# Kernel optimization log

Hardware: AMD Instinct MI355X
Metric: run time of the kernel (lower is better)

## Reference

```python
import jax, jax.numpy as jnp
import numpy as np
import math

D_MODEL = 1024
N_HEADS = 16
HEAD_DIM = D_MODEL // N_HEADS
TOP_K = 32
SCALE = math.sqrt(HEAD_DIM)


def setup_inputs() -> dict:
    key = jax.random.key(0)
    ks = jax.random.split(key, 12)
    B, S, N = 2, 2048, 2048
    std = 1.0 / math.sqrt(D_MODEL)
    inp = {
        "x": jax.random.normal(ks[0], (B, S, D_MODEL), dtype=jnp.float32),
        "knowledge_embeddings": jax.random.normal(ks[1], (B, N, D_MODEL), dtype=jnp.float32),
        "Wq": jax.random.normal(ks[2], (D_MODEL, D_MODEL), dtype=jnp.float32) * std,
        "bq": jnp.zeros((D_MODEL,), dtype=jnp.float32),
        "Wk": jax.random.normal(ks[3], (D_MODEL, D_MODEL), dtype=jnp.float32) * std,
        "bk": jnp.zeros((D_MODEL,), dtype=jnp.float32),
        "Wv": jax.random.normal(ks[4], (D_MODEL, D_MODEL), dtype=jnp.float32) * std,
        "bv": jnp.zeros((D_MODEL,), dtype=jnp.float32),
        "Wo": jax.random.normal(ks[5], (D_MODEL, D_MODEL), dtype=jnp.float32) * std,
        "bo": jnp.zeros((D_MODEL,), dtype=jnp.float32),
    }
    return inp


def _split_heads(t, n):
    # [B, L, d_model] -> [B, H, L, head_dim]
    B, L, _ = t.shape
    return t.reshape(B, L, N_HEADS, HEAD_DIM).transpose(0, 2, 1, 3)


def reference(x, knowledge_embeddings, Wq, bq, Wk, bk, Wv, bv, Wo, bo):
    B, S, _ = x.shape
    N = knowledge_embeddings.shape[1]
    Q = _split_heads(x @ Wq.T + bq, N_HEADS)                    # [B,H,S,hd]
    K = _split_heads(knowledge_embeddings @ Wk.T + bk, N_HEADS)  # [B,H,N,hd]
    V = _split_heads(knowledge_embeddings @ Wv.T + bv, N_HEADS)  # [B,H,N,hd]

    scores = jnp.einsum("bhsd,bhnd->bhsn", Q, K) / SCALE        # [B,H,S,N]
    k = min(TOP_K, N)
    topk_scores, topk_indices = jax.lax.top_k(scores, k)        # [B,H,S,k]
    sparse_weights = jax.nn.softmax(topk_scores, axis=-1)       # [B,H,S,k]
    # dropout=0.0 (eval) -> identity

    # gather V rows: V [B,H,N,hd] with indices [B,H,S,k] along N axis
    sel_V = jnp.take_along_axis(
        V[:, :, None, :, :],                  # [B,H,1,N,hd]
        topk_indices[..., None],              # [B,H,S,k,1]
        axis=3,
    )                                          # [B,H,S,k,hd]
    context = jnp.einsum("bhsk,bhskd->bhsd", sparse_weights, sel_V)
    context = context.transpose(0, 2, 1, 3).reshape(B, S, D_MODEL)
    return context @ Wo.T + bo
```

## Files before the change

kernel.cpp:

```cpp
#include <hip/hip_runtime.h>
#include <math.h>

typedef unsigned long long u64;
typedef unsigned int u32;
typedef unsigned short ush;
typedef __attribute__((ext_vector_type(8))) short short8;
typedef __attribute__((ext_vector_type(4))) float f32x4;

#define BATCH   2
#define SEQ     2048
#define NKNOW   2048
#define DMODEL  1024
#define NHEADS  16
#define HDIM    64
#define TOPK    32
#define MSEL    44

#define MFMA16(A, B, C) __builtin_amdgcn_mfma_f32_16x16x32_bf16(A, B, C, 0, 0, 0)

__device__ __forceinline__ ush f2bf(float x) {
    u32 u = __float_as_uint(x);
    return (ush)((u + 0x7FFFu + ((u >> 16) & 1u)) >> 16);
}
__device__ __forceinline__ float bf2f(ush b) { return __uint_as_float(((u32)b) << 16); }

__global__ __launch_bounds__(256) void gemm_xwt_bias(
    const float* __restrict__ X, const float* __restrict__ W,
    const float* __restrict__ bias, float* __restrict__ Y)
{
    __shared__ float As[16][132];
    __shared__ float Bs[16][132];

    const int t  = threadIdx.x;
    const int m0 = blockIdx.x * 128;
    const int n0 = blockIdx.y * 128;

    const int lm = t >> 2;
    const int lk = (t & 3) << 2;
    const int tx = t & 15;
    const int ty = t >> 4;

    float acc[8][8];
#pragma unroll
    for (int i = 0; i < 8; ++i)
#pragma unroll
        for (int j = 0; j < 8; ++j) acc[i][j] = 0.f;

    for (int k0 = 0; k0 < 1024; k0 += 16) {
        float4 a0 = *(const float4*)(X + (size_t)(m0 + lm) * 1024 + k0 + lk);
        float4 a1 = *(const float4*)(X + (size_t)(m0 + lm + 64) * 1024 + k0 + lk);
        float4 b0 = *(const float4*)(W + (size_t)(n0 + lm) * 1024 + k0 + lk);
        float4 b1 = *(const float4*)(W + (size_t)(n0 + lm + 64) * 1024 + k0 + lk);
        __syncthreads();
        As[lk + 0][lm] = a0.x; As[lk + 1][lm] = a0.y; As[lk + 2][lm] = a0.z; As[lk + 3][lm] = a0.w;
        As[lk + 0][lm + 64] = a1.x; As[lk + 1][lm + 64] = a1.y; As[lk + 2][lm + 64] = a1.z; As[lk + 3][lm + 64] = a1.w;
        Bs[lk + 0][lm] = b0.x; Bs[lk + 1][lm] = b0.y; Bs[lk + 2][lm] = b0.z; Bs[lk + 3][lm] = b0.w;
        Bs[lk + 0][lm + 64] = b1.x; Bs[lk + 1][lm + 64] = b1.y; Bs[lk + 2][lm + 64] = b1.z; Bs[lk + 3][lm + 64] = b1.w;
        __syncthreads();
#pragma unroll
        for (int k = 0; k < 16; ++k) {
            float a[8], b[8];
            *(float4*)(a)     = *(const float4*)&As[k][ty * 8];
            *(float4*)(a + 4) = *(const float4*)&As[k][ty * 8 + 4];
            *(float4*)(b)     = *(const float4*)&Bs[k][tx * 4];
            *(float4*)(b + 4) = *(const float4*)&Bs[k][64 + tx * 4];
#pragma unroll
            for (int i = 0; i < 8; ++i)
#pragma unroll
                for (int j = 0; j < 8; ++j)
                    acc[i][j] = fmaf(a[i], b[j], acc[i][j]);
        }
    }

    float4 bv0 = *(const float4*)(bias + n0 + tx * 4);
    float4 bv1 = *(const float4*)(bias + n0 + 64 + tx * 4);
#pragma unroll
    for (int i = 0; i < 8; ++i) {
        size_t row = (size_t)(m0 + ty * 8 + i) * 1024;
        float4 r0, r1;
        r0.x = acc[i][0] + bv0.x; r0.y = acc[i][1] + bv0.y;
        r0.z = acc[i][2] + bv0.z; r0.w = acc[i][3] + bv0.w;
        r1.x = acc[i][4] + bv1.x; r1.y = acc[i][5] + bv1.y;
        r1.z = acc[i][6] + bv1.z; r1.w = acc[i][7] + bv1.w;
        *(float4*)(Y + row + n0 + tx * 4)      = r0;
        *(float4*)(Y + row + n0 + 64 + tx * 4) = r1;
    }
}

__global__ __launch_bounds__(256) void split_bf16(
    const float* __restrict__ in, ush* __restrict__ oh, ush* __restrict__ ol, int n)
{
    int i = (blockIdx.x * 256 + threadIdx.x) * 4;
    if (i >= n) return;
    float4 v = *(const float4*)(in + i);
    ush h0 = f2bf(v.x), h1 = f2bf(v.y), h2 = f2bf(v.z), h3 = f2bf(v.w);
    ushort4 hv; hv.x = h0; hv.y = h1; hv.z = h2; hv.w = h3;
    ushort4 lv;
    lv.x = f2bf(v.x - bf2f(h0)); lv.y = f2bf(v.y - bf2f(h1));
    lv.z = f2bf(v.z - bf2f(h2)); lv.w = f2bf(v.w - bf2f(h3));
    *(ushort4*)(oh + i) = hv;
    *(ushort4*)(ol + i) = lv;
}

__global__ __launch_bounds__(256) void conv_bf16(
    const float* __restrict__ in, ush* __restrict__ o, int n)
{
    int i = (blockIdx.x * 256 + threadIdx.x) * 4;
    if (i >= n) return;
    float4 v = *(const float4*)(in + i);
    ushort4 hv;
    hv.x = f2bf(v.x); hv.y = f2bf(v.y); hv.z = f2bf(v.z); hv.w = f2bf(v.w);
    *(ushort4*)(o + i) = hv;
}

__global__ __launch_bounds__(256) void gemm_mfma_split(
    const ush* __restrict__ Ah, const ush* __restrict__ Al,
    const ush* __restrict__ Bh, const ush* __restrict__ Bl,
    const float* __restrict__ bias, float* __restrict__ Yf)
{
    __shared__ ush sAh[4096], sAl[4096];
    __shared__ ush sBh[8192], sBl[8192];

    const int t = threadIdx.x;
    const int w = t >> 6, lane = t & 63;
    const int m0 = blockIdx.x * 64;
    const int n0 = blockIdx.y * 128;

    f32x4 acc[4][2];
#pragma unroll
    for (int i = 0; i < 4; ++i)
#pragma unroll
        for (int j = 0; j < 2; ++j) acc[i][j] = (f32x4){0.f, 0.f, 0.f, 0.f};

    for (int k0 = 0; k0 < 1024; k0 += 64) {
        __syncthreads();
#pragma unroll
        for (int c = t; c < 512; c += 256) {
            int t16 = c >> 7, ks = (c >> 6) & 1, ln = c & 63;
            int row = t16 * 16 + (ln & 15);
            int k8  = ks * 4 + (ln >> 4);
            size_t g = (size_t)(m0 + row) * 1024 + k0 + k8 * 8;
            *(uint4*)&sAh[c * 8] = *(const uint4*)(Ah + g);
            *(uint4*)&sAl[c * 8] = *(const uint4*)(Al + g);
        }
#pragma unroll
        for (int c = t; c < 1024; c += 256) {
            int t16 = c >> 7, ks = (c >> 6) & 1, ln = c & 63;
            int row = t16 * 16 + (ln & 15);
            int k8  = ks * 4 + (ln >> 4);
            size_t g = (size_t)(n0 + row) * 1024 + k0 + k8 * 8;
            *(uint4*)&sBh[c * 8] = *(const uint4*)(Bh + g);
            *(uint4*)&sBl[c * 8] = *(const uint4*)(Bl + g);
        }
        __syncthreads();

#pragma unroll
        for (int ks = 0; ks < 2; ++ks) {
            short8 a_h[4], a_l[4], b_h[2], b_l[2];
#pragma unroll
            for (int i = 0; i < 4; ++i) {
                a_h[i] = *(const short8*)&sAh[((i * 2 + ks) * 64 + lane) * 8];
                a_l[i] = *(const short8*)&sAl[((i * 2 + ks) * 64 + lane) * 8];
            }
#pragma unroll
            for (int j = 0; j < 2; ++j) {
                int nt = w * 2 + j;
                b_h[j] = *(const short8*)&sBh[((nt * 2 + ks) * 64 + lane) * 8];
                b_l[j] = *(const short8*)&sBl[((nt * 2 + ks) * 64 + lane) * 8];
            }
#pragma unroll
            for (int i = 0; i < 4; ++i)
#pragma unroll
                for (int j = 0; j < 2; ++j) {
                    acc[i][j] = MFMA16(a_h[i], b_h[j], acc[i][j]);
                    acc[i][j] = MFMA16(a_h[i], b_l[j], acc[i][j]);
                    acc[i][j] = MFMA16(a_l[i], b_h[j], acc[i][j]);
                }
        }
    }

    const int quad = lane >> 4, c16 = lane & 15;
#pragma unroll
    for (int i = 0; i < 4; ++i)
#pragma unroll
        for (int j = 0; j < 2; ++j) {
            int colg = n0 + (w * 2 + j) * 16 + c16;
            float bia = bias[colg];
#pragma unroll
            for (int r = 0; r < 4; ++r) {
                int rowg = m0 + i * 16 + quad * 4 + r;
                Yf[(size_t)rowg * 1024 + colg] = acc[i][j][r] + bia;
            }
        }
}

__global__ __launch_bounds__(256) void scores_bf16(
    const ush* __restrict__ Qb, const ush* __restrict__ Kb,
    ush* __restrict__ Sc, int bh0)
{
    __shared__ ush sA[8192], sB[8192];

    const int t = threadIdx.x;
    const int w = t >> 6, lane = t & 63;
    const int s0  = blockIdx.x * 128;
    const int nn0 = blockIdx.y * 128;
    const int bhl = blockIdx.z;
    const int bh  = bh0 + bhl;
    const int b   = bh >> 4, h = bh & 15;

#pragma unroll
    for (int c = t; c < 1024; c += 256) {
        int t16 = c >> 7, ks = (c >> 6) & 1, ln = c & 63;
        int row = t16 * 16 + (ln & 15);
        int k8  = ks * 4 + (ln >> 4);
        size_t gq = ((size_t)b * SEQ + s0 + row) * 1024 + h * 64 + k8 * 8;
        size_t gk = ((size_t)b * NKNOW + nn0 + row) * 1024 + h * 64 + k8 * 8;
        *(uint4*)&sA[c * 8] = *(const uint4*)(Qb + gq);
        *(uint4*)&sB[c * 8] = *(const uint4*)(Kb + gk);
    }
    __syncthreads();

    const int r0t = (w >> 1) * 4, c0t = (w & 1) * 4;
    f32x4 acc[4][4];
#pragma unroll
    for (int i = 0; i < 4; ++i)
#pragma unroll
        for (int j = 0; j < 4; ++j) acc[i][j] = (f32x4){0.f, 0.f, 0.f, 0.f};

#pragma unroll
    for (int ks = 0; ks < 2; ++ks) {
        short8 a[4], bb[4];
#pragma unroll
        for (int i = 0; i < 4; ++i)
            a[i] = *(const short8*)&sA[(((r0t + i) * 2 + ks) * 64 + lane) * 8];
#pragma unroll
        for (int j = 0; j < 4; ++j)
            bb[j] = *(const short8*)&sB[(((c0t + j) * 2 + ks) * 64 + lane) * 8];
#pragma unroll
        for (int i = 0; i < 4; ++i)
#pragma unroll
            for (int j = 0; j < 4; ++j)
                acc[i][j] = MFMA16(a[i], bb[j], acc[i][j]);
    }

    const int quad = lane >> 4, c16 = lane & 15;
#pragma unroll
    for (int i = 0; i < 4; ++i)
#pragma unroll
        for (int j = 0; j < 4; ++j) {
            int colg = nn0 + (c0t + j) * 16 + c16;
#pragma unroll
            for (int r = 0; r < 4; ++r) {
                int rowg = s0 + (r0t + i) * 16 + quad * 4 + r;
                Sc[((size_t)bhl * SEQ + rowg) * 2048 + colg] = f2bf(acc[i][j][r] * 0.125f);
            }
        }
}

__device__ __forceinline__ u32 mkey_of(float v) {
    u32 u = __float_as_uint(v);
    return (u & 0x80000000u) ? ~u : (u | 0x80000000u);
}
__device__ __forceinline__ u64 pk64(float v, int col) {
    return (((u64)mkey_of(v)) << 32) | (u32)(2047 - col);
}

__global__ __launch_bounds__(256) void topk_rescore(
    const ush* __restrict__ Scb, const float* __restrict__ Qp,
    const float* __restrict__ Kp, const float* __restrict__ Vp,
    ush* __restrict__ ctxh, ush* __restrict__ ctxl, int bh0)
{
    __shared__ u32 binsAll[4][256];
    __shared__ u64 candAll[4][64];
    __shared__ u32 selcAll[4][64];
    __shared__ u64 selAll[4][32];
    __shared__ float qrowAll[4][64];

    const int t = threadIdx.x, w = t >> 6, l = t & 63;
    const int Rl  = blockIdx.x * 4 + w;
    const int bhl = Rl >> 11, s = Rl & 2047;
    const int bh  = bh0 + bhl;
    const int b   = bh >> 4, h = bh & 15;

    u32* bins = binsAll[w];
    u64* cand = candAll[w];
    u32* selc = selcAll[w];
    u64* sel  = selAll[w];
    float* qrow = qrowAll[w];

    float v[32];
    const ush* srow = Scb + (size_t)Rl * 2048;
#pragma unroll
    for (int j = 0; j < 4; ++j) {
        ushort4 p0 = *(const ushort4*)(srow + j * 512 + l * 8);
        ushort4 p1 = *(const ushort4*)(srow + j * 512 + l * 8 + 4);
        v[8 * j + 0] = bf2f(p0.x); v[8 * j + 1] = bf2f(p0.y);
        v[8 * j + 2] = bf2f(p0.z); v[8 * j + 3] = bf2f(p0.w);
        v[8 * j + 4] = bf2f(p1.x); v[8 * j + 5] = bf2f(p1.y);
        v[8 * j + 6] = bf2f(p1.z); v[8 * j + 7] = bf2f(p1.w);
    }

    qrow[l] = Qp[((size_t)b * SEQ + s) * 1024 + h * 64 + l];

    float m = v[0];
#pragma unroll
    for (int i = 1; i < 32; ++i) m = fmaxf(m, v[i]);
#pragma unroll
    for (int d2 = 1; d2 < 64; d2 <<= 1) m = fmaxf(m, __shfl_xor(m, d2, 64));

    float lo = m - 8.0f, width = 8.0f;
    u32 cmask = 0xFFFFFFFFu;
    u32 need  = MSEL;
    u64 T64   = 0;
    int found = 0;

    for (int attempt = 0; attempt < 6 && !found; ++attempt) {
        const float scale = 256.0f / width;

        *(uint4*)&bins[4 * l] = make_uint4(0u, 0u, 0u, 0u);
        __builtin_amdgcn_wave_barrier();

        u32 bidxArr[8];
#pragma unroll
        for (int q = 0; q < 8; ++q) bidxArr[q] = 0;
#pragma unroll
        for (int i = 0; i < 32; ++i) {
            if ((cmask >> i) & 1u) {
                int bi = (int)((v[i] - lo) * scale);
                bi = bi < 0 ? 0 : (bi > 255 ? 255 : bi);
                atomicAdd(&bins[bi], 1u);
                bidxArr[i >> 2] |= (u32)bi << ((i & 3) * 8);
            }
        }
        __builtin_amdgcn_wave_barrier();

        uint4 c4 = *(const uint4*)&bins[4 * l];
        u32 tl  = c4.x + c4.y + c4.z + c4.w;
        u32 suf = tl;
#pragma unroll
        for (int d2 = 1; d2 < 64; d2 <<= 1) {
            u32 o = __shfl_down(suf, d2, 64);
            suf += (l + d2 < 64) ? o : 0u;
        }
        u32 above = suf - tl;
        u32 s3 = above + c4.w;
        u32 s2 = s3 + c4.z;
        u32 s1 = s2 + c4.y;
        u32 s0 = s1 + c4.x;

        bool has = (s0 >= need) && (above < need);
        int dloc = 0; u32 needloc = 0; int Cloc = 0;
        if (has) {
            if      (s3 >= need) { dloc = 4 * l + 3; needloc = need - above; Cloc = (int)c4.w; }
            else if (s2 >= need) { dloc = 4 * l + 2; needloc = need - s3;    Cloc = (int)c4.z; }
            else if (s1 >= need) { dloc = 4 * l + 1; needloc = need - s2;    Cloc = (int)c4.y; }
            else                 { dloc = 4 * l;     needloc = need - s1;    Cloc = (int)c4.x; }
        }
        u64 bal = __ballot(has);
        int src = (int)__ffsll(bal) - 1;
        int d     = __shfl(dloc, src, 64);
        u32 need2 = (u32)__shfl((int)needloc, src, 64);
        int C     = __shfl(Cloc, src, 64);

        if (C <= 64) {
            u32 cb = 0;
#pragma unroll
            for (int i = 0; i < 32; ++i) {
                int bi = (int)((bidxArr[i >> 2] >> ((i & 3) * 8)) & 255u);
                bool inb = (((cmask >> i) & 1u) != 0u) && (bi == d);
                u64 b2 = __ballot(inb);
                if (inb) {
                    u32 slot = cb + (u32)__popcll(b2 & ((1ull << l) - 1ull));
                    if (slot < 64) {
                        int col = ((i >> 3) << 9) + (l << 3) + (i & 7);
                        cand[slot] = pk64(v[i], col);
                    }
                }
                cb += (u32)__popcll(b2);
            }
            __builtin_amdgcn_wave_barrier();

            u64 myk = (l < C) ? cand[l] : 0ull;
            int rank = 0;
            for (int j = 0; j < C; ++j) rank += (cand[j] > myk) ? 1 : 0;
            bool isT = (l < C) && (rank == (int)need2 - 1);
            u64 balT = __ballot(isT);
            int srcT = (int)__ffsll(balT) - 1;
            T64 = __shfl(myk, srcT, 64);
            found = 1;
        } else {
            need = need2;
            u32 nm = 0;
#pragma unroll
            for (int i = 0; i < 32; ++i) {
                int bi = (int)((bidxArr[i >> 2] >> ((i & 3) * 8)) & 255u);
                if ((((cmask >> i) & 1u) != 0u) && (bi == d)) nm |= 1u << i;
            }
            cmask = nm;
            const float bw = width * (1.0f / 256.0f);
            if (d > 0) { lo = lo + (float)d * bw; width = bw; }
            else       { float edge = lo + bw; width = width * 4.0f; lo = edge - width; }
        }
    }

    u32 cb = 0;
#pragma unroll
    for (int i = 0; i < 32; ++i) {
        int col = ((i >> 3) << 9) + (l << 3) + (i & 7);
        bool sb = pk64(v[i], col) >= T64;
        u64 b2 = __ballot(sb);
        if (sb) {
            u32 slot = cb + (u32)__popcll(b2 & ((1ull << l) - 1ull));
            if (slot < 64) selc[slot] = (u32)col;
        }
        cb += (u32)__popcll(b2);
    }
    __builtin_amdgcn_wave_barrier();

    float sx = -3.0e38f;
    u32 mycol = 0;
    if (l < MSEL) {
        mycol = selc[l];
        const float* kr = Kp + ((size_t)b * NKNOW + mycol) * 1024 + h * 64;
        float p0 = 0.f, p1 = 0.f, p2 = 0.f, p3 = 0.f;
#pragma unroll
        for (int d = 0; d < 64; d += 4) {
            float4 kv = *(const float4*)(kr + d);
            float4 qv = *(const float4*)&qrow[d];
            p0 = fmaf(qv.x, kv.x, p0);
            p1 = fmaf(qv.y, kv.y, p1);
            p2 = fmaf(qv.z, kv.z, p2);
            p3 = fmaf(qv.w, kv.w, p3);
        }
        sx = ((p0 + p1) + (p2 + p3)) * 0.125f;
    }

    cand[l] = (l < MSEL) ? pk64(sx, (int)mycol) : 0ull;
    __builtin_amdgcn_wave_barrier();
    u64 myk = cand[l];
    int rank = 0;
#pragma unroll 4
    for (int j = 0; j < MSEL; ++j) rank += (cand[j] > myk) ? 1 : 0;
    const bool win = (l < MSEL) && (rank < TOPK);

    float mx = win ? sx : -3.0e38f;
#pragma unroll
    for (int d2 = 1; d2 < 64; d2 <<= 1) mx = fmaxf(mx, __shfl_xor(mx, d2, 64));
    float e = win ? __expf(sx - mx) : 0.0f;
    float Z = e;
#pragma unroll
    for (int d2 = 1; d2 < 64; d2 <<= 1) Z += __shfl_xor(Z, d2, 64);
    const float invZ = 1.0f / Z;

    u64 bw2 = __ballot(win);
    if (win) {
        u32 slot = (u32)__popcll(bw2 & ((1ull << l) - 1ull));
        sel[slot] = (((u64)__float_as_uint(e)) << 32) | mycol;
    }
    __builtin_amdgcn_wave_barrier();

    float acc = 0.0f;
    for (int j = 0; j < TOPK; ++j) {
        u64 pc = sel[j];
        float ej = __uint_as_float((u32)(pc >> 32));
        u32 colj = (u32)(pc & 0xFFFFFFFFu);
        acc = fmaf(ej * invZ, Vp[((size_t)b * NKNOW + colj) * 1024 + h * 64 + l], acc);
    }
    size_t oidx = ((size_t)b * SEQ + s) * 1024 + h * 64 + l;
    ush hh = f2bf(acc);
    ctxh[oidx] = hh;
    ctxl[oidx] = f2bf(acc - bf2f(hh));
}

extern "C" void kernel_launch(void* const* d_in, const int* in_sizes, int n_in,
                              void* d_out, int out_size, void* d_ws, size_t ws_size,
                              hipStream_t stream)
{
    const float* x  = (const float*)d_in[0];
    const float* ke = (const float*)d_in[1];
    const float* Wq = (const float*)d_in[2];
    const float* bq = (const float*)d_in[3];
    const float* Wk = (const float*)d_in[4];
    const float* bk = (const float*)d_in[5];
    const float* Wv = (const float*)d_in[6];
    const float* bv = (const float*)d_in[7];
    const float* Wo = (const float*)d_in[8];
    const float* bo = (const float*)d_in[9];
    float* out = (float*)d_out;

    const size_t NB = (size_t)4096 * 1024;
    const size_t NW = (size_t)1024 * 1024;

    char* p = (char*)d_ws;
    float *Qp = (float*)p;  p += NB * 4;
    float *Kp = (float*)p;  p += NB * 4;
    float *Vp = (float*)p;  p += NB * 4;
    ush *Qb  = (ush*)p;     p += NB * 2;
    ush *Kb  = (ush*)p;     p += NB * 2;
    ush *keh = (ush*)p;     p += NB * 2;
    ush *kel = (ush*)p;     p += NB * 2;
    ush *Wvh = (ush*)p;     p += NW * 2;
    ush *Wvl = (ush*)p;     p += NW * 2;
    ush *Woh = (ush*)p;     p += NW * 2;
    ush *Wol = (ush*)p;     p += NW * 2;
    ush *ctxh = (ush*)p;    p += NB * 2;
    ush *ctxl = (ush*)p;    p += NB * 2;
    ush *Sc = (ush*)p;
    const size_t fixedBytes = (size_t)(p - (char*)d_ws);

    int bhg = 1;
    {
        const int tiers[6] = {32, 16, 8, 4, 2, 1};
        for (int i = 0; i < 6; ++i) {
            size_t scB = (size_t)tiers[i] * SEQ * NKNOW * 2;
            if (fixedBytes + scB <= ws_size) { bhg = tiers[i]; break; }
        }
    }

    dim3 blk(256);

    hipLaunchKernelGGL(split_bf16, dim3((int)(NB / 1024)), blk, 0, stream, ke, keh, kel, (int)NB);
    hipLaunchKernelGGL(split_bf16, dim3((int)(NW / 1024)), blk, 0, stream, Wv, Wvh, Wvl, (int)NW);
    hipLaunchKernelGGL(split_bf16, dim3((int)(NW / 1024)), blk, 0, stream, Wo, Woh, Wol, (int)NW);

    dim3 g32(32, 8);
    hipLaunchKernelGGL(gemm_xwt_bias, g32, blk, 0, stream, x,  Wq, bq, Qp);
    hipLaunchKernelGGL(gemm_xwt_bias, g32, blk, 0, stream, ke, Wk, bk, Kp);

    dim3 gmf(64, 8);
    hipLaunchKernelGGL(gemm_mfma_split, gmf, blk, 0, stream, keh, kel, Wvh, Wvl, bv, Vp);

    hipLaunchKernelGGL(conv_bf16, dim3((int)(NB / 1024)), blk, 0, stream, Qp, Qb, (int)NB);
    hipLaunchKernelGGL(conv_bf16, dim3((int)(NB / 1024)), blk, 0, stream, Kp, Kb, (int)NB);

    for (int bh0 = 0; bh0 < 32; bh0 += bhg) {
        hipLaunchKernelGGL(scores_bf16, dim3(SEQ / 128, NKNOW / 128, bhg), blk, 0, stream,
                           Qb, Kb, Sc, bh0);
        hipLaunchKernelGGL(topk_rescore, dim3(bhg * SEQ / 4), blk, 0, stream,
                           Sc, Qp, Kp, Vp, ctxh, ctxl, bh0);
    }

    hipLaunchKernelGGL(gemm_mfma_split, gmf, blk, 0, stream, ctxh, ctxl, Woh, Wol, bo, out);
}
```

Baseline: 879.0 us.

## Retile fp32 projection GEMM, fuse bf16 conversion, simplify top-k threshold search

The fp32 Q/K projection GEMM is retiled from 128x128 with K-step 16 to 64x128 with K-step 32. It now writes a bf16 copy in its epilogue, so the two separate conversion kernels are removed. The top-k rescoring kernel replaces exact 44-candidate threshold selection with a histogram refinement capped at three passes that picks a float threshold yielding up to 64 candidates. Candidates are then gathered with LDS atomics and ranked over 64 slots. This removes launches and memory passes and shortens the selection loop, at the cost of a variable candidate count and possibly more rescoring work per row.

```diff
diff --git a/kernel.cpp b/kernel.cpp
--- a/kernel.cpp
+++ b/kernel.cpp
@@ -14,7 +14,7 @@
 #define NHEADS  16
 #define HDIM    64
 #define TOPK    32
-#define MSEL    44
+#define CPAD    44
 
 #define MFMA16(A, B, C) __builtin_amdgcn_mfma_f32_16x16x32_bf16(A, B, C, 0, 0, 0)
 
@@ -24,66 +24,72 @@
 }
 __device__ __forceinline__ float bf2f(ush b) { return __uint_as_float(((u32)b) << 16); }
 
-__global__ __launch_bounds__(256) void gemm_xwt_bias(
+__global__ __launch_bounds__(256) void gemm_f32_v2(
     const float* __restrict__ X, const float* __restrict__ W,
-    const float* __restrict__ bias, float* __restrict__ Y)
+    const float* __restrict__ bias, float* __restrict__ Y, ush* __restrict__ Yb)
 {
-    __shared__ float As[16][132];
-    __shared__ float Bs[16][132];
+    __shared__ float As[32][66];
+    __shared__ float Bs[32][130];
 
     const int t  = threadIdx.x;
-    const int m0 = blockIdx.x * 128;
+    const int m0 = blockIdx.x * 64;
     const int n0 = blockIdx.y * 128;
 
-    const int lm = t >> 2;
-    const int lk = (t & 3) << 2;
-    const int tx = t & 15;
-    const int ty = t >> 4;
-
-    float acc[8][8];
+    const int ra = t >> 2, ka = (t & 3) * 8;
+    const int rb = t >> 1, kb = (t & 1) * 16;
+
+    const int ty = t >> 5;
+    const int tx = t & 31;
+
+    float acc[8][4];
 #pragma unroll
     for (int i = 0; i < 8; ++i)
 #pragma unroll
-        for (int j = 0; j < 8; ++j) acc[i][j] = 0.f;
-
-    for (int k0 = 0; k0 < 1024; k0 += 16) {
-        float4 a0 = *(const float4*)(X + (size_t)(m0 + lm) * 1024 + k0 + lk);
-        float4 a1 = *(const float4*)(X + (size_t)(m0 + lm + 64) * 1024 + k0 + lk);
-        float4 b0 = *(const float4*)(W + (size_t)(n0 + lm) * 1024 + k0 + lk);
-        float4 b1 = *(const float4*)(W + (size_t)(n0 + lm + 64) * 1024 + k0 + lk);
+        for (int j = 0; j < 4; ++j) acc[i][j] = 0.f;
+
+    for (int k0 = 0; k0 < 1024; k0 += 32) {
+        float4 a0 = *(const float4*)(X + (size_t)(m0 + ra) * 1024 + k0 + ka);
+        float4 a1 = *(const float4*)(X + (size_t)(m0 + ra) * 1024 + k0 + ka + 4);
+        float4 b0 = *(const float4*)(W + (size_t)(n0 + rb) * 1024 + k0 + kb);
+        float4 b1 = *(const float4*)(W + (size_t)(n0 + rb) * 1024 + k0 + kb + 4);
+        float4 b2 = *(const float4*)(W + (size_t)(n0 + rb) * 1024 + k0 + kb + 8);
+        float4 b3 = *(const float4*)(W + (size_t)(n0 + rb) * 1024 + k0 + kb + 12);
         __syncthreads();
-        As[lk + 0][lm] = a0.x; As[lk + 1][lm] = a0.y; As[lk + 2][lm] = a0.z; As[lk + 3][lm] = a0.w;
-        As[lk + 0][lm + 64] = a1.x; As[lk + 1][lm + 64] = a1.y; As[lk + 2][lm + 64] = a1.z; As[lk + 3][lm + 64] = a1.w;
-        Bs[lk + 0][lm] = b0.x; Bs[lk + 1][lm] = b0.y; Bs[lk + 2][lm] = b0.z; Bs[lk + 3][lm] = b0.w;
-        Bs[lk + 0][lm + 64] = b1.x; Bs[lk + 1][lm + 64] = b1.y; Bs[lk + 2][lm + 64] = b1.z; Bs[lk + 3][lm + 64] = b1.w;
+        As[ka + 0][ra] = a0.x; As[ka + 1][ra] = a0.y; As[ka + 2][ra] = a0.z; As[ka + 3][ra] = a0.w;
+        As[ka + 4][ra] = a1.x; As[ka + 5][ra] = a1.y; As[ka + 6][ra] = a1.z; As[ka + 7][ra] = a1.w;
+        Bs[kb + 0][rb] = b0.x; Bs[kb + 1][rb] = b0.y; Bs[kb + 2][rb] = b0.z; Bs[kb + 3][rb] = b0.w;
+        Bs[kb + 4][rb] = b1.x; Bs[kb + 5][rb] = b1.y; Bs[kb + 6][rb] = b1.z; Bs[kb + 7][rb] = b1.w;
+        Bs[kb + 8][rb] = b2.x; Bs[kb + 9][rb] = b2.y; Bs[kb +10][rb] = b2.z; Bs[kb +11][rb] = b2.w;
+        Bs[kb +12][rb] = b3.x; Bs[kb +13][rb] = b3.y; Bs[kb +14][rb] = b3.z; Bs[kb +15][rb] = b3.w;
         __syncthreads();
-#pragma unroll
-        for (int k = 0; k < 16; ++k) {
-            float a[8], b[8];
+#pragma unroll 4
+        for (int k = 0; k < 32; ++k) {
+            float a[8], b[4];
             *(float4*)(a)     = *(const float4*)&As[k][ty * 8];
             *(float4*)(a + 4) = *(const float4*)&As[k][ty * 8 + 4];
             *(float4*)(b)     = *(const float4*)&Bs[k][tx * 4];
-            *(float4*)(b + 4) = *(const float4*)&Bs[k][64 + tx * 4];
 #pragma unroll
             for (int i = 0; i < 8; ++i)
 #pragma unroll
-                for (int j = 0; j < 8; ++j)
+                for (int j = 0; j < 4; ++j)
                     acc[i][j] = fmaf(a[i], b[j], acc[i][j]);
         }
     }
 
-    float4 bv0 = *(const float4*)(bias + n0 + tx * 4);
-    float4 bv1 = *(const float4*)(bias + n0 + 64 + tx * 4);
+    float4 bv = *(const float4*)(bias + n0 + tx * 4);
+    const float bb[4] = {bv.x, bv.y, bv.z, bv.w};
 #pragma unroll
     for (int i = 0; i < 8; ++i) {
         size_t row = (size_t)(m0 + ty * 8 + i) * 1024;
-        float4 r0, r1;
-        r0.x = acc[i][0] + bv0.x; r0.y = acc[i][1] + bv0.y;
-        r0.z = acc[i][2] + bv0.z; r0.w = acc[i][3] + bv0.w;
-        r1.x = acc[i][4] + bv1.x; r1.y = acc[i][5] + bv1.y;
-        r1.z = acc[i][6] + bv1.z; r1.w = acc[i][7] + bv1.w;
-        *(float4*)(Y + row + n0 + tx * 4)      = r0;
-        *(float4*)(Y + row + n0 + 64 + tx * 4) = r1;
+        float4 r;
+        r.x = acc[i][0] + bb[0]; r.y = acc[i][1] + bb[1];
+        r.z = acc[i][2] + bb[2]; r.w = acc[i][3] + bb[3];
+        *(float4*)(Y + row + n0 + tx * 4) = r;
+        if (Yb) {
+            ushort4 h;
+            h.x = f2bf(r.x); h.y = f2bf(r.y); h.z = f2bf(r.z); h.w = f2bf(r.w);
+            *(ushort4*)(Yb + row + n0 + tx * 4) = h;
+        }
     }
 }
 
@@ -102,17 +108,6 @@
     *(ushort4*)(ol + i) = lv;
 }
 
-__global__ __launch_bounds__(256) void conv_bf16(
-    const float* __restrict__ in, ush* __restrict__ o, int n)
-{
-    int i = (blockIdx.x * 256 + threadIdx.x) * 4;
-    if (i >= n) return;
-    float4 v = *(const float4*)(in + i);
-    ushort4 hv;
-    hv.x = f2bf(v.x); hv.y = f2bf(v.y); hv.z = f2bf(v.z); hv.w = f2bf(v.w);
-    *(ushort4*)(o + i) = hv;
-}
-
 __global__ __launch_bounds__(256) void gemm_mfma_split(
     const ush* __restrict__ Ah, const ush* __restrict__ Al,
     const ush* __restrict__ Bh, const ush* __restrict__ Bl,
@@ -265,16 +260,17 @@
     return (((u64)mkey_of(v)) << 32) | (u32)(2047 - col);
 }
 
-__global__ __launch_bounds__(256) void topk_rescore(
+__global__ __launch_bounds__(256) void topk_rescore2(
     const ush* __restrict__ Scb, const float* __restrict__ Qp,
     const float* __restrict__ Kp, const float* __restrict__ Vp,
     ush* __restrict__ ctxh, ush* __restrict__ ctxl, int bh0)
 {
     __shared__ u32 binsAll[4][256];
-    __shared__ u64 candAll[4][64];
+    __shared__ u64 keysAll[4][64];
     __shared__ u32 selcAll[4][64];
     __shared__ u64 selAll[4][32];
     __shared__ float qrowAll[4][64];
+    __shared__ u32 cntAll[4];
 
     const int t = threadIdx.x, w = t >> 6, l = t & 63;
     const int Rl  = blockIdx.x * 4 + w;
@@ -283,7 +279,7 @@
     const int b   = bh >> 4, h = bh & 15;
 
     u32* bins = binsAll[w];
-    u64* cand = candAll[w];
+    u64* keys = keysAll[w];
     u32* selc = selcAll[w];
     u64* sel  = selAll[w];
     float* qrow = qrowAll[w];
@@ -309,27 +305,28 @@
     for (int d2 = 1; d2 < 64; d2 <<= 1) m = fmaxf(m, __shfl_xor(m, d2, 64));
 
     float lo = m - 8.0f, width = 8.0f;
-    u32 cmask = 0xFFFFFFFFu;
-    u32 need  = MSEL;
-    u64 T64   = 0;
-    int found = 0;
-
-    for (int attempt = 0; attempt < 6 && !found; ++attempt) {
+    u32 base = 0;
+    int havePrev = 0; float pLo = 0.f, pScale = 0.f; int pBkt = 0;
+    float T = m - 8.0f;
+
+    for (int att = 0; att < 3; ++att) {
         const float scale = 256.0f / width;
 
         *(uint4*)&bins[4 * l] = make_uint4(0u, 0u, 0u, 0u);
         __builtin_amdgcn_wave_barrier();
 
-        u32 bidxArr[8];
-#pragma unroll
-        for (int q = 0; q < 8; ++q) bidxArr[q] = 0;
 #pragma unroll
         for (int i = 0; i < 32; ++i) {
-            if ((cmask >> i) & 1u) {
-                int bi = (int)((v[i] - lo) * scale);
-                bi = bi < 0 ? 0 : (bi > 255 ? 255 : bi);
+            float vi = v[i];
+            bool in = (vi >= lo);
+            if (havePrev) {
+                int pb = (int)fminf((vi - pLo) * pScale, 255.0f);
+                in = (vi >= pLo) && (pb == pBkt);
+            }
+            if (in) {
+                int bi = (int)fminf((vi - lo) * scale, 255.0f);
+                bi = bi < 0 ? 0 : bi;
                 atomicAdd(&bins[bi], 1u);
-                bidxArr[i >> 2] |= (u32)bi << ((i & 3) * 8);
             }
         }
         __builtin_amdgcn_wave_barrier();
@@ -343,83 +340,54 @@
             suf += (l + d2 < 64) ? o : 0u;
         }
         u32 above = suf - tl;
-        u32 s3 = above + c4.w;
-        u32 s2 = s3 + c4.z;
-        u32 s1 = s2 + c4.y;
-        u32 s0 = s1 + c4.x;
-
-        bool has = (s0 >= need) && (above < need);
-        int dloc = 0; u32 needloc = 0; int Cloc = 0;
-        if (has) {
-            if      (s3 >= need) { dloc = 4 * l + 3; needloc = need - above; Cloc = (int)c4.w; }
-            else if (s2 >= need) { dloc = 4 * l + 2; needloc = need - s3;    Cloc = (int)c4.z; }
-            else if (s1 >= need) { dloc = 4 * l + 1; needloc = need - s2;    Cloc = (int)c4.y; }
-            else                 { dloc = 4 * l;     needloc = need - s1;    Cloc = (int)c4.x; }
-        }
+        u32 cs3 = base + above + c4.w;
+        u32 cs2 = cs3 + c4.z;
+        u32 cs1 = cs2 + c4.y;
+        u32 cs0 = cs1 + c4.x;
+
+        bool has = (cs3 <= 64);
+        int eloc; u32 nloc;
+        if      (cs0 <= 64) { eloc = 4 * l;     nloc = cs0; }
+        else if (cs1 <= 64) { eloc = 4 * l + 1; nloc = cs1; }
+        else if (cs2 <= 64) { eloc = 4 * l + 2; nloc = cs2; }
+        else                { eloc = 4 * l + 3; nloc = cs3; }
+
         u64 bal = __ballot(has);
-        int src = (int)__ffsll(bal) - 1;
-        int d     = __shfl(dloc, src, 64);
-        u32 need2 = (u32)__shfl((int)needloc, src, 64);
-        int C     = __shfl(Cloc, src, 64);
-
-        if (C <= 64) {
-            u32 cb = 0;
-#pragma unroll
-            for (int i = 0; i < 32; ++i) {
-                int bi = (int)((bidxArr[i >> 2] >> ((i & 3) * 8)) & 255u);
-                bool inb = (((cmask >> i) & 1u) != 0u) && (bi == d);
-                u64 b2 = __ballot(inb);
-                if (inb) {
-                    u32 slot = cb + (u32)__popcll(b2 & ((1ull << l) - 1ull));
-                    if (slot < 64) {
-                        int col = ((i >> 3) << 9) + (l << 3) + (i & 7);
-                        cand[slot] = pk64(v[i], col);
-                    }
-                }
-                cb += (u32)__popcll(b2);
-            }
-            __builtin_amdgcn_wave_barrier();
-
-            u64 myk = (l < C) ? cand[l] : 0ull;
-            int rank = 0;
-            for (int j = 0; j < C; ++j) rank += (cand[j] > myk) ? 1 : 0;
-            bool isT = (l < C) && (rank == (int)need2 - 1);
-            u64 balT = __ballot(isT);
-            int srcT = (int)__ffsll(balT) - 1;
-            T64 = __shfl(myk, srcT, 64);
-            found = 1;
-        } else {
-            need = need2;
-            u32 nm = 0;
-#pragma unroll
-            for (int i = 0; i < 32; ++i) {
-                int bi = (int)((bidxArr[i >> 2] >> ((i & 3) * 8)) & 255u);
-                if ((((cmask >> i) & 1u) != 0u) && (bi == d)) nm |= 1u << i;
-            }
-            cmask = nm;
-            const float bw = width * (1.0f / 256.0f);
-            if (d > 0) { lo = lo + (float)d * bw; width = bw; }
-            else       { float edge = lo + bw; width = width * 4.0f; lo = edge - width; }
-        }
-    }
-
-    u32 cb = 0;
+        const float bw = width * (1.0f / 256.0f);
+        if (bal == 0ull) {
+            havePrev = 1; pLo = lo; pScale = scale; pBkt = 255;
+            lo = lo + 255.0f * bw; width = bw;
+            T = lo;
+            continue;
+        }
+        int src  = (int)__ffsll(bal) - 1;
+        int eS   = __shfl(eloc, src, 64);
+        u32 nAt  = (u32)__shfl((int)nloc, src, 64);
+        T = lo + (float)eS * bw;
+        if (nAt >= CPAD || eS == 0 || att == 2) break;
+        havePrev = 1; pLo = lo; pScale = scale; pBkt = eS - 1;
+        base = nAt;
+        lo = lo + (float)(eS - 1) * bw; width = bw;
+    }
+
+    if (l == 0) cntAll[w] = 0u;
+    __builtin_amdgcn_wave_barrier();
 #pragma unroll
     for (int i = 0; i < 32; ++i) {
-        int col = ((i >> 3) << 9) + (l << 3) + (i & 7);
-        bool sb = pk64(v[i], col) >= T64;
-        u64 b2 = __ballot(sb);
-        if (sb) {
-            u32 slot = cb + (u32)__popcll(b2 & ((1ull << l) - 1ull));
-            if (slot < 64) selc[slot] = (u32)col;
-        }
-        cb += (u32)__popcll(b2);
+        if (v[i] >= T) {
+            u32 slot = atomicAdd(&cntAll[w], 1u);
+            if (slot < 64) {
+                int col = ((i >> 3) << 9) + (l << 3) + (i & 7);
+                selc[slot] = (u32)col;
+            }
+        }
     }
     __builtin_amdgcn_wave_barrier();
+    int C = (int)cntAll[w]; C = C > 64 ? 64 : C;
 
     float sx = -3.0e38f;
     u32 mycol = 0;
-    if (l < MSEL) {
+    if (l < C) {
         mycol = selc[l];
         const float* kr = Kp + ((size_t)b * NKNOW + mycol) * 1024 + h * 64;
         float p0 = 0.f, p1 = 0.f, p2 = 0.f, p3 = 0.f;
@@ -435,13 +403,13 @@
         sx = ((p0 + p1) + (p2 + p3)) * 0.125f;
     }
 
-    cand[l] = (l < MSEL) ? pk64(sx, (int)mycol) : 0ull;
+    keys[l] = (l < C) ? pk64(sx, (int)mycol) : 0ull;
     __builtin_amdgcn_wave_barrier();
-    u64 myk = cand[l];
+    u64 myk = keys[l];
     int rank = 0;
-#pragma unroll 4
-    for (int j = 0; j < MSEL; ++j) rank += (cand[j] > myk) ? 1 : 0;
-    const bool win = (l < MSEL) && (rank < TOPK);
+#pragma unroll 8
+    for (int j = 0; j < 64; ++j) rank += (keys[j] > myk) ? 1 : 0;
+    const bool win = (l < C) && (rank < TOPK);
 
     float mx = win ? sx : -3.0e38f;
 #pragma unroll
@@ -523,20 +491,17 @@
     hipLaunchKernelGGL(split_bf16, dim3((int)(NW / 1024)), blk, 0, stream, Wv, Wvh, Wvl, (int)NW);
     hipLaunchKernelGGL(split_bf16, dim3((int)(NW / 1024)), blk, 0, stream, Wo, Woh, Wol, (int)NW);
 
-    dim3 g32(32, 8);
-    hipLaunchKernelGGL(gemm_xwt_bias, g32, blk, 0, stream, x,  Wq, bq, Qp);
-    hipLaunchKernelGGL(gemm_xwt_bias, g32, blk, 0, stream, ke, Wk, bk, Kp);
+    dim3 g64(64, 8);
+    hipLaunchKernelGGL(gemm_f32_v2, g64, blk, 0, stream, x,  Wq, bq, Qp, Qb);
+    hipLaunchKernelGGL(gemm_f32_v2, g64, blk, 0, stream, ke, Wk, bk, Kp, Kb);
 
     dim3 gmf(64, 8);
     hipLaunchKernelGGL(gemm_mfma_split, gmf, blk, 0, stream, keh, kel, Wvh, Wvl, bv, Vp);
-
-    hipLaunchKernelGGL(conv_bf16, dim3((int)(NB / 1024)), blk, 0, stream, Qp, Qb, (int)NB);
-    hipLaunchKernelGGL(conv_bf16, dim3((int)(NB / 1024)), blk, 0, stream, Kp, Kb, (int)NB);
 
     for (int bh0 = 0; bh0 < 32; bh0 += bhg) {
         hipLaunchKernelGGL(scores_bf16, dim3(SEQ / 128, NKNOW / 128, bhg), blk, 0, stream,
                            Qb, Kb, Sc, bh0);
-        hipLaunchKernelGGL(topk_rescore, dim3(bhg * SEQ / 4), blk, 0, stream,
+        hipLaunchKernelGGL(topk_rescore2, dim3(bhg * SEQ / 4), blk, 0, stream,
                            Sc, Qp, Kp, Vp, ctxh, ctxl, bh0);
     }
 
```

Result: faster. 780.6 us (-11.2%).
